# Performance work log

Hardware: AMD Instinct MI355X
Metric: run time of the kernel (lower is better)

Reference implementation:

```python
import jax, jax.numpy as jnp
import numpy as np

N_EMBD = 1024
HEAD_SIZE = 64
BLOCK_SIZE = 512
BATCH = 4


def setup_inputs() -> dict:
    key = jax.random.key(0)
    ks = jax.random.split(key, 5)
    T = BLOCK_SIZE
    x = jax.random.normal(ks[0], (BATCH, 2 * T - 1, N_EMBD), dtype=jnp.float32)
    scale = 1.0 / np.sqrt(N_EMBD)
    Wk = jax.random.normal(ks[1], (N_EMBD, HEAD_SIZE), dtype=jnp.float32) * scale
    Wv = jax.random.normal(ks[2], (N_EMBD, HEAD_SIZE), dtype=jnp.float32) * scale
    Wq = jax.random.normal(ks[3], (N_EMBD, HEAD_SIZE), dtype=jnp.float32) * scale
    # keyWindowBias in torch has shape (1,1,head_size,block_size); store as (hs, T)
    bias = jax.random.normal(ks[4], (HEAD_SIZE, T), dtype=jnp.float32)
    return {"x": x, "Wk": Wk, "Wv": Wv, "Wq": Wq, "bias": bias}


def reference(x, Wk, Wv, Wq, bias):
    B, S, C = x.shape
    T = (S + 1) // 2  # S == 2*T - 1 (block_size)
    xToPred = x[:, -T:, :]
    # block_layer == 0 path: project full sequence for k, v
    k = jnp.einsum('bsc,cd->bsd', x, Wk)        # [B, 2T-1, hs]
    v = jnp.einsum('bsc,cd->bsd', x, Wv)        # [B, 2T-1, hs]
    q = jnp.einsum('btc,cd->btd', xToPred, Wq)  # [B, T, hs]

    # sliding windows: window w covers positions w..w+T-1 (torch unfold semantics)
    idx = jnp.arange(T)[:, None] + jnp.arange(T)[None, :]  # [T, T]

    k_win = k[:, idx, :] + bias.T[None, None, :, :]  # [B, T, T, hs] + [1,1,T,hs]
    wei = jnp.einsum('bwd,bwtd->bwt', q, k_win)      # [B, T, T]
    wei = jax.nn.softmax(wei, axis=-1)

    v_win = v[:, idx, :]                              # [B, T, T, hs]
    out = jnp.einsum('bwt,bwtd->bwd', wei, v_win)     # [B, T, hs]
    return out
```

## Files before the change

kernel.cpp:

```cpp
#include <hip/hip_runtime.h>
#include <hip/hip_bf16.h>

#define BB 4
#define SS 1023
#define TT 512
#define CC 1024
#define DD 64
#define NROW (BB*SS)
#define NROWP 4096

typedef float f4 __attribute__((ext_vector_type(4)));
typedef float f2 __attribute__((ext_vector_type(2)));
typedef short bf16x8 __attribute__((ext_vector_type(8)));
typedef short s4 __attribute__((ext_vector_type(4)));
typedef float f32x4 __attribute__((ext_vector_type(4)));

__device__ __forceinline__ unsigned split_rtn(float v) {
    const unsigned u  = __builtin_bit_cast(unsigned, v);
    const unsigned r  = u + 0x7FFFu + ((u >> 16) & 1u);
    const unsigned hi = r >> 16;
    const float hif   = __builtin_bit_cast(float, r & 0xFFFF0000u);
    const float res   = v - hif;
    const unsigned u2 = __builtin_bit_cast(unsigned, res);
    const unsigned r2 = u2 + 0x7FFFu + ((u2 >> 16) & 1u);
    return (r2 & 0xFFFF0000u) | hi;
}

__global__ __launch_bounds__(64) void wsplit_kernel(
    const float* __restrict__ Wk,
    const float* __restrict__ Wv,
    const float* __restrict__ Wq,
    unsigned short* __restrict__ bwh,
    unsigned short* __restrict__ bwl)
{
    const int f    = blockIdx.x;
    const int p    = f >> 7;
    const int rem  = f & 127;
    const int nsub = rem >> 5;
    const int ks   = rem & 31;
    const int lane = threadIdx.x;
    const int quad = lane >> 4, l4 = lane & 15;
    const float* W = (p == 0) ? Wk : (p == 1) ? Wv : Wq;
    const int n = nsub * 16 + l4;

    bf16x8 h, l;
#pragma unroll
    for (int j = 0; j < 8; ++j) {
        const int k = ks * 32 + quad * 8 + j;
        const unsigned hl = split_rtn(W[k * DD + n]);
        h[j] = (short)(hl & 0xFFFFu);
        l[j] = (short)(hl >> 16);
    }
    ((bf16x8*)bwh)[f * 64 + lane] = h;
    ((bf16x8*)bwl)[f * 64 + lane] = l;
}

__global__ __launch_bounds__(256) void proj_fused_kernel(
    const float* __restrict__ x,
    const unsigned short* __restrict__ bwh,
    const unsigned short* __restrict__ bwl,
    float* __restrict__ kT,
    float* __restrict__ vbuf,
    float* __restrict__ qbuf)
{
    __shared__ __align__(16) unsigned short lh[16 * 1024];
    __shared__ __align__(16) unsigned short ll[16 * 1024];

    const int blk  = blockIdx.x;
    const int p    = blk % 3;
    const int mt   = blk / 3;
    const int bs0  = mt * 16;
    const int tid  = threadIdx.x;

    {
        const int k = tid * 4;
#pragma unroll 4
        for (int i = 0; i < 16; ++i) {
            int arow = bs0 + i; if (arow > NROW - 1) arow = NROW - 1;
            const f4 xv = *(const f4*)(x + (size_t)arow * CC + k);
            s4 h, l;
#pragma unroll
            for (int j = 0; j < 4; ++j) {
                const unsigned hl = split_rtn(xv[j]);
                h[j] = (short)(hl & 0xFFFFu);
                l[j] = (short)(hl >> 16);
            }
            const int idx = i * 1024 + (k ^ ((i & 7) << 3));
            *(s4*)&lh[idx] = h;
            *(s4*)&ll[idx] = l;
        }
    }
    __syncthreads();

    const int lane = tid & 63;
    const int w    = tid >> 6;
    const int quad = lane >> 4, l4 = lane & 15;

    const bf16x8* bh = (const bf16x8*)bwh
                     + (size_t)((p * 4 + w) * 32) * 64 + lane;
    const bf16x8* bl = (const bf16x8*)bwl
                     + (size_t)((p * 4 + w) * 32) * 64 + lane;

    const int rbase = l4 * 1024;
    const int kxor  = (l4 & 7) << 3;

    f32x4 acc = {0.f, 0.f, 0.f, 0.f};
#pragma unroll 4
    for (int ks = 0; ks < 32; ++ks) {
        const int k0 = ks * 32 + quad * 8;
        const bf16x8 ah = *(const bf16x8*)&lh[rbase + (k0 ^ kxor)];
        const bf16x8 al = *(const bf16x8*)&ll[rbase + (k0 ^ kxor)];
        const bf16x8 bhn = bh[ks * 64];
        const bf16x8 bln = bl[ks * 64];
        acc = __builtin_amdgcn_mfma_f32_16x16x32_bf16(ah, bhn, acc, 0, 0, 0);
        acc = __builtin_amdgcn_mfma_f32_16x16x32_bf16(ah, bln, acc, 0, 0, 0);
        acc = __builtin_amdgcn_mfma_f32_16x16x32_bf16(al, bhn, acc, 0, 0, 0);
        acc = __builtin_amdgcn_mfma_f32_16x16x32_bf16(al, bln, acc, 0, 0, 0);
    }

    {
        const int d = w * 16 + l4;
#pragma unroll
        for (int reg = 0; reg < 4; ++reg) {
            const int bs = bs0 + quad * 4 + reg;
            if (bs < NROW) {
                const float val = acc[reg];
                const int b = bs / SS, ss = bs - b * SS;
                if (p == 0) {
                    kT[(size_t)d * NROWP + b * 1024 + ss] = val;
                } else if (p == 1) {
                    vbuf[(size_t)bs * DD + d] = val;
                } else {
                    if (ss >= TT - 1)
                        qbuf[((size_t)b * TT + (ss - (TT - 1))) * DD + d] = val;
                }
            }
        }
    }
}

__global__ __launch_bounds__(512) void attn_kernel(
    const float* __restrict__ kT,
    const float* __restrict__ vbuf,
    const float* __restrict__ qbuf,
    const float* __restrict__ bias,
    float* __restrict__ out)
{
    __shared__ __align__(8) float qsT[DD][2];
    __shared__ __align__(8) float part[2][2][TT];
    __shared__ __align__(8) float weiT[TT][2];
    __shared__ float red[16];
    __shared__ float invs[2];
    __shared__ float partial[8][2][DD];

    const int tid  = threadIdx.x;
    const int lane = tid & 63;
    const int wv   = tid >> 6;
    const int blk  = blockIdx.x;
    const int b    = blk >> 8;
    const int w0   = (blk & 255) * 2;

    if (tid < 2 * DD) {
        const int m = tid >> 6, dd = tid & 63;
        qsT[dd][m] = qbuf[((size_t)b * TT + w0 + m) * DD + dd];
    }
    __syncthreads();

    {
        const int h = tid >> 8, p = tid & 255;
        const int t0 = 2 * p;
        const float* kcol = kT + (size_t)(32 * h) * NROWP + b * 1024 + w0 + t0;
        const float* bp   = bias + (size_t)(32 * h) * TT + t0;
        float a00 = 0.f, a01 = 0.f, a10 = 0.f, a11 = 0.f;
#pragma unroll 8
        for (int i = 0; i < 32; ++i) {
            const float* kr = kcol + (size_t)i * NROWP;
            const f2 kA = *(const f2*)kr;
            const float kC = kr[2];
            const f2 bv = *(const f2*)(bp + (size_t)i * TT);
            const f2 qv = *(const f2*)&qsT[32 * h + i][0];
            a00 = fmaf(qv[0], kA[0], a00);
            a01 = fmaf(qv[0], kA[1], a01);
            a10 = fmaf(qv[1], kA[1], a10);
            a11 = fmaf(qv[1], kC,    a11);
            a00 = fmaf(qv[0], bv[0], a00);
            a01 = fmaf(qv[0], bv[1], a01);
            a10 = fmaf(qv[1], bv[0], a10);
            a11 = fmaf(qv[1], bv[1], a11);
        }
        *(f2*)&part[h][0][t0] = (f2){a00, a01};
        *(f2*)&part[h][1][t0] = (f2){a10, a11};
    }
    __syncthreads();

    {
        const int m = wv >> 2, qt = wv & 3;
        const int tb = qt * 128 + lane;
        float r0 = part[0][m][tb]      + part[1][m][tb];
        float r1 = part[0][m][tb + 64] + part[1][m][tb + 64];
        float mx = fmaxf(r0, r1);
#pragma unroll
        for (int off = 1; off < 64; off <<= 1)
            mx = fmaxf(mx, __shfl_xor(mx, off, 64));
        if (lane == 0) red[wv] = mx;
        __syncthreads();
        mx = fmaxf(fmaxf(red[m * 4], red[m * 4 + 1]),
                   fmaxf(red[m * 4 + 2], red[m * 4 + 3]));
        const float e0 = __expf(r0 - mx), e1 = __expf(r1 - mx);
        weiT[tb][m] = e0;
        weiT[tb + 64][m] = e1;
        float sum = e0 + e1;
#pragma unroll
        for (int off = 1; off < 64; off <<= 1)
            sum += __shfl_xor(sum, off, 64);
        if (lane == 0) red[8 + wv] = sum;
        __syncthreads();
        if (tid < 2)
            invs[tid] = 1.f / (red[8 + tid * 4] + red[9 + tid * 4] +
                               red[10 + tid * 4] + red[11 + tid * 4]);
    }
    __syncthreads();

    {
        const int t0r = wv * 64;
        const float* vb = vbuf + ((size_t)b * SS + w0 + t0r) * DD + lane;
        float p0 = 0.f, p1 = 0.f;
        float v0 = vb[0];
#pragma unroll 4
        for (int t = 0; t < 64; ++t) {
            const float v1 = vb[(size_t)(t + 1) * DD];
            const f2 w2 = *(const f2*)&weiT[t0r + t][0];
            p0 = fmaf(w2[0], v0, p0);
            p1 = fmaf(w2[1], v1, p1);
            v0 = v1;
        }
        partial[wv][0][lane] = p0;
        partial[wv][1][lane] = p1;
    }
    __syncthreads();

    if (tid < 2 * DD) {
        const int m = tid >> 6, dd = tid & 63;
        float o = 0.f;
#pragma unroll
        for (int j = 0; j < 8; ++j) o += partial[j][m][dd];
        out[((size_t)b * TT + w0 + m) * DD + dd] = o * invs[m];
    }
}

extern "C" void kernel_launch(void* const* d_in, const int* in_sizes, int n_in,
                              void* d_out, int out_size, void* d_ws, size_t ws_size,
                              hipStream_t stream) {
    const float* x    = (const float*)d_in[0];
    const float* Wk   = (const float*)d_in[1];
    const float* Wv   = (const float*)d_in[2];
    const float* Wq   = (const float*)d_in[3];
    const float* bias = (const float*)d_in[4];
    float* out = (float*)d_out;

    char* ws = (char*)d_ws;
    float* kT             = (float*)(ws + 0);
    float* vbuf           = (float*)(ws + (2u  << 20));
    float* qbuf           = (float*)(ws + (4u  << 20));
    unsigned short* bwh   = (unsigned short*)(ws + (6u  << 20));
    unsigned short* bwl   = (unsigned short*)(ws + (8u  << 20));

    wsplit_kernel<<<384, 64, 0, stream>>>(Wk, Wv, Wq, bwh, bwl);
    proj_fused_kernel<<<768, 256, 0, stream>>>(x, bwh, bwl, kT, vbuf, qbuf);
    attn_kernel<<<BB * TT / 2, 512, 0, stream>>>(kT, vbuf, qbuf, bias, out);
}
```

Before: 115.4 us.

## Process eight query windows per attention block to reuse K/V/bias loads

Each attention block now handles eight consecutive windows instead of two, so every loaded K column, bias value and V row is reused across eight windows through shifted register windows. The grid shrinks fourfold, and the softmax reduction becomes one wavefront per window, which removes the cross-wave max/sum exchange and two barriers. In exchange each thread holds more accumulators (higher register pressure), shared memory use grows, and only 256 blocks are launched, which may underfill the GPU.

Result: faster. 107.4 us (-6.9%).

```diff
diff --git a/kernel.cpp b/kernel.cpp
--- a/kernel.cpp
+++ b/kernel.cpp
@@ -146,21 +146,20 @@
     const float* __restrict__ bias,
     float* __restrict__ out)
 {
-    __shared__ __align__(8) float qsT[DD][2];
-    __shared__ __align__(8) float part[2][2][TT];
-    __shared__ __align__(8) float weiT[TT][2];
-    __shared__ float red[16];
-    __shared__ float invs[2];
-    __shared__ float partial[8][2][DD];
+    __shared__ __align__(16) float qsT[DD][8];
+    __shared__ __align__(8) float part[2][8][TT];
+    __shared__ float weiT[TT][9];
+    __shared__ float invs[8];
+    __shared__ float partial[8][8][DD];
 
     const int tid  = threadIdx.x;
     const int lane = tid & 63;
     const int wv   = tid >> 6;
     const int blk  = blockIdx.x;
-    const int b    = blk >> 8;
-    const int w0   = (blk & 255) * 2;
-
-    if (tid < 2 * DD) {
+    const int b    = blk >> 6;
+    const int w0   = (blk & 63) * 8;
+
+    if (tid < 8 * DD) {
         const int m = tid >> 6, dd = tid & 63;
         qsT[dd][m] = qbuf[((size_t)b * TT + w0 + m) * DD + dd];
     }
@@ -171,75 +170,92 @@
         const int t0 = 2 * p;
         const float* kcol = kT + (size_t)(32 * h) * NROWP + b * 1024 + w0 + t0;
         const float* bp   = bias + (size_t)(32 * h) * TT + t0;
-        float a00 = 0.f, a01 = 0.f, a10 = 0.f, a11 = 0.f;
-#pragma unroll 8
+        float am[8][2];
+#pragma unroll
+        for (int m = 0; m < 8; ++m) { am[m][0] = 0.f; am[m][1] = 0.f; }
+#pragma unroll 4
         for (int i = 0; i < 32; ++i) {
             const float* kr = kcol + (size_t)i * NROWP;
-            const f2 kA = *(const f2*)kr;
-            const float kC = kr[2];
+            const f2 k01 = *(const f2*)kr;
+            const f2 k23 = *(const f2*)(kr + 2);
+            const f2 k45 = *(const f2*)(kr + 4);
+            const f2 k67 = *(const f2*)(kr + 6);
+            const float k8 = kr[8];
             const f2 bv = *(const f2*)(bp + (size_t)i * TT);
-            const f2 qv = *(const f2*)&qsT[32 * h + i][0];
-            a00 = fmaf(qv[0], kA[0], a00);
-            a01 = fmaf(qv[0], kA[1], a01);
-            a10 = fmaf(qv[1], kA[1], a10);
-            a11 = fmaf(qv[1], kC,    a11);
-            a00 = fmaf(qv[0], bv[0], a00);
-            a01 = fmaf(qv[0], bv[1], a01);
-            a10 = fmaf(qv[1], bv[0], a10);
-            a11 = fmaf(qv[1], bv[1], a11);
-        }
-        *(f2*)&part[h][0][t0] = (f2){a00, a01};
-        *(f2*)&part[h][1][t0] = (f2){a10, a11};
-    }
-    __syncthreads();
-
-    {
-        const int m = wv >> 2, qt = wv & 3;
-        const int tb = qt * 128 + lane;
-        float r0 = part[0][m][tb]      + part[1][m][tb];
-        float r1 = part[0][m][tb + 64] + part[1][m][tb + 64];
-        float mx = fmaxf(r0, r1);
+            const f4 qA = *(const f4*)&qsT[32 * h + i][0];
+            const f4 qB = *(const f4*)&qsT[32 * h + i][4];
+            const float kk[9] = {k01[0], k01[1], k23[0], k23[1],
+                                 k45[0], k45[1], k67[0], k67[1], k8};
+            const float qq[8] = {qA[0], qA[1], qA[2], qA[3],
+                                 qB[0], qB[1], qB[2], qB[3]};
+#pragma unroll
+            for (int m = 0; m < 8; ++m) {
+                am[m][0] = fmaf(qq[m], kk[m],     am[m][0]);
+                am[m][0] = fmaf(qq[m], bv[0],     am[m][0]);
+                am[m][1] = fmaf(qq[m], kk[m + 1], am[m][1]);
+                am[m][1] = fmaf(qq[m], bv[1],     am[m][1]);
+            }
+        }
+#pragma unroll
+        for (int m = 0; m < 8; ++m)
+            *(f2*)&part[h][m][t0] = (f2){am[m][0], am[m][1]};
+    }
+    __syncthreads();
+
+    {
+        const int m = wv;
+        float r[8];
+#pragma unroll
+        for (int j = 0; j < 8; ++j) {
+            const int t = lane + 64 * j;
+            r[j] = part[0][m][t] + part[1][m][t];
+        }
+        float mx = r[0];
+#pragma unroll
+        for (int j = 1; j < 8; ++j) mx = fmaxf(mx, r[j]);
 #pragma unroll
         for (int off = 1; off < 64; off <<= 1)
             mx = fmaxf(mx, __shfl_xor(mx, off, 64));
-        if (lane == 0) red[wv] = mx;
-        __syncthreads();
-        mx = fmaxf(fmaxf(red[m * 4], red[m * 4 + 1]),
-                   fmaxf(red[m * 4 + 2], red[m * 4 + 3]));
-        const float e0 = __expf(r0 - mx), e1 = __expf(r1 - mx);
-        weiT[tb][m] = e0;
-        weiT[tb + 64][m] = e1;
-        float sum = e0 + e1;
+        float sum = 0.f;
+#pragma unroll
+        for (int j = 0; j < 8; ++j) {
+            const float e = __expf(r[j] - mx);
+            weiT[lane + 64 * j][m] = e;
+            sum += e;
+        }
 #pragma unroll
         for (int off = 1; off < 64; off <<= 1)
             sum += __shfl_xor(sum, off, 64);
-        if (lane == 0) red[8 + wv] = sum;
-        __syncthreads();
-        if (tid < 2)
-            invs[tid] = 1.f / (red[8 + tid * 4] + red[9 + tid * 4] +
-                               red[10 + tid * 4] + red[11 + tid * 4]);
+        if (lane == 0) invs[m] = 1.f / sum;
     }
     __syncthreads();
 
     {
         const int t0r = wv * 64;
         const float* vb = vbuf + ((size_t)b * SS + w0 + t0r) * DD + lane;
-        float p0 = 0.f, p1 = 0.f;
-        float v0 = vb[0];
-#pragma unroll 4
+        float pm[8];
+#pragma unroll
+        for (int m = 0; m < 8; ++m) pm[m] = 0.f;
+        float vv[8];
+#pragma unroll
+        for (int m = 0; m < 7; ++m) vv[m] = vb[(size_t)m * DD];
+#pragma unroll 2
         for (int t = 0; t < 64; ++t) {
-            const float v1 = vb[(size_t)(t + 1) * DD];
-            const f2 w2 = *(const f2*)&weiT[t0r + t][0];
-            p0 = fmaf(w2[0], v0, p0);
-            p1 = fmaf(w2[1], v1, p1);
-            v0 = v1;
-        }
-        partial[wv][0][lane] = p0;
-        partial[wv][1][lane] = p1;
-    }
-    __syncthreads();
-
-    if (tid < 2 * DD) {
+            vv[7] = vb[(size_t)(t + 7) * DD];
+            const float* wt = &weiT[t0r + t][0];
+#pragma unroll
+            for (int m = 0; m < 8; ++m)
+                pm[m] = fmaf(wt[m], vv[m], pm[m]);
+#pragma unroll
+            for (int m = 0; m < 7; ++m) vv[m] = vv[m + 1];
+        }
+#pragma unroll
+        for (int m = 0; m < 8; ++m)
+            partial[wv][m][lane] = pm[m];
+    }
+    __syncthreads();
+
+    {
         const int m = tid >> 6, dd = tid & 63;
         float o = 0.f;
 #pragma unroll
@@ -267,5 +283,5 @@
 
     wsplit_kernel<<<384, 64, 0, stream>>>(Wk, Wv, Wq, bwh, bwl);
     proj_fused_kernel<<<768, 256, 0, stream>>>(x, bwh, bwl, kT, vbuf, qbuf);
-    attn_kernel<<<BB * TT / 2, 512, 0, stream>>>(kT, vbuf, qbuf, bias, out);
-}
+    attn_kernel<<<BB * TT / 8, 512, 0, stream>>>(kT, vbuf, qbuf, bias, out);
+}
```
